# Performance work log

Measured on AMD Instinct MI355X. Metric: run time of the kernel, lower is better.

The kernel has to match this reference:

```python
import jax, jax.numpy as jnp
import numpy as np

B, T, I, H = 64, 1024, 256, 512


def setup_inputs() -> dict:
    key = jax.random.key(0)
    ks = jax.random.split(key, 5)
    s = 1.0 / np.sqrt(H)  # PyTorch LSTM init scale (uniform(-s, s)); we use scaled normal
    return {
        "x": jax.random.normal(ks[0], (B, T, I), dtype=jnp.float32),
        "w_ih": jax.random.normal(ks[1], (4 * H, I), dtype=jnp.float32) * s,
        "w_hh": jax.random.normal(ks[2], (4 * H, H), dtype=jnp.float32) * s,
        "b_ih": jax.random.normal(ks[3], (4 * H,), dtype=jnp.float32) * s,
        "b_hh": jax.random.normal(ks[4], (4 * H,), dtype=jnp.float32) * s,
    }


def _lstm(x, w_ih, w_hh, b_ih, b_hh):
    # x: [B, T, I]. Precompute input projections for all timesteps at once.
    pre = jnp.einsum("bti,gi->btg", x, w_ih) + b_ih + b_hh  # [B, T, 4H]
    pre = jnp.swapaxes(pre, 0, 1)  # [T, B, 4H] for scan over time

    h0 = jnp.zeros((x.shape[0], H), dtype=x.dtype)
    c0 = jnp.zeros((x.shape[0], H), dtype=x.dtype)

    def step(carry, pre_t):
        h, c = carry
        gates = pre_t + h @ w_hh.T  # [B, 4H]
        i, f, g, o = jnp.split(gates, 4, axis=-1)  # PyTorch gate order: i, f, g, o
        i = jax.nn.sigmoid(i)
        f = jax.nn.sigmoid(f)
        g = jnp.tanh(g)
        o = jax.nn.sigmoid(o)
        c = f * c + i * g
        h = o * jnp.tanh(c)
        return (h, c), h

    (h_n, c_n), hs = jax.lax.scan(step, (h0, c0), pre)
    out = jnp.swapaxes(hs, 0, 1)  # [B, T, H] (batch_first=True)
    return out, (h_n[None], c_n[None])  # h_n/c_n: [num_layers=1, B, H]


def reference(x, w_ih, w_hh, b_ih, b_hh):
    return _lstm(x, w_ih, w_hh, b_ih, b_hh)
```

## Files before the change

kernel.cpp:

```cpp
#include <hip/hip_runtime.h>
#include <cstdint>
#include <cstddef>


#define NBATCH 64
#define TSTEPS 1024
#define IDIM   256
#define HDIM   512
#define KDIM   768
#define WS     776
#define ABUF_USHORT (16 * WS)
#define BIAS_OFF    (2 * ABUF_USHORT * 2)
#define SMEM_BYTES  (BIAS_OFF + 1024)

#define HB_WORDS 32768

typedef __attribute__((ext_vector_type(8))) short short8x;
typedef __attribute__((ext_vector_type(4))) float f32x4;
typedef __attribute__((ext_vector_type(4))) unsigned int u32x4;

__device__ __forceinline__ float sigmoid_f(float v) {
    return 1.0f / (1.0f + __expf(-v));
}
__device__ __forceinline__ float tanh_f(float v) {
    float a = fabsf(v);
    float e = __expf(-2.0f * a);
    float r = (1.0f - e) / (1.0f + e);
    return v >= 0.0f ? r : -r;
}
__device__ __forceinline__ unsigned short f2bf(float f) {
    unsigned int u = __float_as_uint(f);
    return (unsigned short)((u + 0x7fffu + ((u >> 16) & 1u)) >> 16);
}
__device__ __forceinline__ unsigned long long pack4(float4 v) {
    unsigned long long b0 = f2bf(v.x), b1 = f2bf(v.y), b2 = f2bf(v.z), b3 = f2bf(v.w);
    return b0 | (b1 << 16) | (b2 << 32) | (b3 << 48);
}
__device__ __forceinline__ unsigned int pklo(unsigned int a, unsigned int b) {
    return (a & 0xffffu) | (b << 16);
}

__global__ void __launch_bounds__(256, 1) lstm_persistent(
    const float* __restrict__ x,
    const float* __restrict__ w_ih,
    const float* __restrict__ w_hh,
    const float* __restrict__ b_ih,
    const float* __restrict__ b_hh,
    float* __restrict__ out,
    unsigned int* __restrict__ h_tb)
{
    const int tid = threadIdx.x;
    const int wg  = blockIdx.x;
    const int bg  = wg >> 3;
    const int hg  = wg & 7;

    extern __shared__ char smem[];
    unsigned short* a0 = (unsigned short*)smem;
    unsigned short* a1 = a0 + ABUF_USHORT;
    float* bias_s = (float*)(smem + BIAS_OFF);

    const int wv   = tid >> 6;
    const int lane = tid & 63;
    const int ln   = lane & 15;
    const int q    = lane >> 4;

    short8x af0[24], af1[24], af2[24], af3[24];
    {
        const int grb = (ln & 3) * HDIM + hg * 64 + wv * 16 + (ln >> 2) * 4;
#define LOADW(AF, TAU)                                                        \
        {                                                                     \
            const int gr = grb + (TAU);                                       \
            _Pragma("unroll")                                                 \
            for (int s = 0; s < 24; ++s) {                                    \
                const float* src = (s < 8)                                    \
                    ? (w_ih + (size_t)gr * IDIM + (s * 32 + q * 8))           \
                    : (w_hh + (size_t)gr * HDIM + ((s - 8) * 32 + q * 8));    \
                float4 v0 = *(const float4*)(src);                            \
                float4 v1 = *(const float4*)(src + 4);                        \
                union { short8x v; unsigned long long u[2]; } tmp;            \
                tmp.u[0] = pack4(v0);                                         \
                tmp.u[1] = pack4(v1);                                         \
                AF[s] = tmp.v;                                                \
            }                                                                 \
        }
        LOADW(af0, 0) LOADW(af1, 1) LOADW(af2, 2) LOADW(af3, 3)
#undef LOADW
    }

    if (ln < 4) {
        const int tau = ln;
        const int hid = hg * 64 + wv * 16 + q * 4 + tau;
        #pragma unroll
        for (int j = 0; j < 4; ++j)
            bias_s[(wv * 4 + q) * 16 + tau * 4 + j] =
                b_ih[j * HDIM + hid] + b_hh[j * HDIM + hid];
    }

    const int sn  = tid >> 4;
    const int sj  = tid & 15;
    const int gbn = bg * 16 + sn;
    const float* xbase = x + (size_t)gbn * TSTEPS * IDIM + sj * 16;

    const size_t hb_off = (size_t)(bg * 16 + ln) * HDIM + hg * 64 + wv * 16 + q * 4;
    float c0 = 0.f, c1 = 0.f, c2 = 0.f, c3 = 0.f;
    float hf0 = 0.f, hf1 = 0.f, hf2 = 0.f, hf3 = 0.f;

    for (int t = 0; t < TSTEPS; ++t) {
        unsigned short* abuf = (t & 1) ? a1 : a0;
        unsigned short* axp  = abuf + sn * WS + sj * 16;
        unsigned int*   ahp32 = (unsigned int*)(abuf + sn * WS + IDIM + sj * 32);

        {
            const float* xp = xbase + (size_t)t * IDIM;
            float4 v0 = *(const float4*)(xp);
            float4 v1 = *(const float4*)(xp + 4);
            float4 v2 = *(const float4*)(xp + 8);
            float4 v3 = *(const float4*)(xp + 12);
            *(unsigned long long*)(axp + 0)  = pack4(v0);
            *(unsigned long long*)(axp + 4)  = pack4(v1);
            *(unsigned long long*)(axp + 8)  = pack4(v2);
            *(unsigned long long*)(axp + 12) = pack4(v3);
        }

        if (t > 0) {
            const unsigned int* hp =
                h_tb + (size_t)(t & 1) * HB_WORDS + (size_t)gbn * HDIM + sj * 32;
            u32x4 hv[8];
            const unsigned int tagw = (unsigned int)t << 16;
            unsigned pend = 0xffu;
            while (pend) {
                #pragma unroll
                for (int u = 0; u < 8; ++u) {
                    if (pend & (1u << u)) {
                        asm volatile("global_load_dwordx4 %0, %1, off sc0 sc1"
                                     : "=v"(hv[u]) : "v"(hp + u * 4) : "memory");
                    }
                }
                asm volatile("s_waitcnt vmcnt(0)" ::: "memory");
                __builtin_amdgcn_sched_barrier(0);
                unsigned np = 0;
                #pragma unroll
                for (int u = 0; u < 8; ++u) {
                    if (pend & (1u << u)) {
                        unsigned m = ((hv[u][0] ^ tagw) | (hv[u][1] ^ tagw) |
                                      (hv[u][2] ^ tagw) | (hv[u][3] ^ tagw))
                                     & 0xffff0000u;
                        if (m) np |= (1u << u);
                    }
                }
                pend = np;
            }
            #pragma unroll
            for (int v = 0; v < 4; ++v) {
                u32x4 a = hv[2 * v], b = hv[2 * v + 1];
                u32x4 w4;
                w4[0] = pklo(a[0], a[1]);
                w4[1] = pklo(a[2], a[3]);
                w4[2] = pklo(b[0], b[1]);
                w4[3] = pklo(b[2], b[3]);
                *(u32x4*)(ahp32 + 4 * v) = w4;
            }
            if ((sn & 7) == ((hg + t) & 7)) {
                float* op = out + ((size_t)gbn * TSTEPS + (t - 1)) * HDIM + sj * 32;
                #pragma unroll
                for (int u = 0; u < 8; ++u) {
                    u32x4 h4 = hv[u];
                    f32x4 f4;
                    f4[0] = __uint_as_float(h4[0] << 16);
                    f4[1] = __uint_as_float(h4[1] << 16);
                    f4[2] = __uint_as_float(h4[2] << 16);
                    f4[3] = __uint_as_float(h4[3] << 16);
                    __builtin_nontemporal_store(f4, (f32x4*)(op + 4 * u));
                }
            }
        } else {
            u32x4 z = {0u, 0u, 0u, 0u};
            #pragma unroll
            for (int v = 0; v < 4; ++v) *(u32x4*)(ahp32 + 4 * v) = z;
        }
        __syncthreads();

        const unsigned short* Bbase = abuf + (size_t)ln * WS + q * 8;
        f32x4 ac0 = {0.f, 0.f, 0.f, 0.f};
        f32x4 ac1 = {0.f, 0.f, 0.f, 0.f};
        f32x4 ac2 = {0.f, 0.f, 0.f, 0.f};
        f32x4 ac3 = {0.f, 0.f, 0.f, 0.f};
        #pragma unroll
        for (int s = 0; s < 24; ++s) {
            short8x bf = *(const short8x*)(Bbase + s * 32);
            ac0 = __builtin_amdgcn_mfma_f32_16x16x32_bf16(af0[s], bf, ac0, 0, 0, 0);
            ac1 = __builtin_amdgcn_mfma_f32_16x16x32_bf16(af1[s], bf, ac1, 0, 0, 0);
            ac2 = __builtin_amdgcn_mfma_f32_16x16x32_bf16(af2[s], bf, ac2, 0, 0, 0);
            ac3 = __builtin_amdgcn_mfma_f32_16x16x32_bf16(af3[s], bf, ac3, 0, 0, 0);
        }

        const unsigned int tagw1 = (unsigned int)(t + 1) << 16;
        const float* bsl = bias_s + (wv * 4 + q) * 16;
        u32x4 pub;
#define ACT(ACC, TAU, CREF, HREF)                                             \
        {                                                                     \
            f32x4 bs = *(const f32x4*)(bsl + (TAU) * 4);                      \
            float ig = sigmoid_f(ACC[0] + bs[0]);                             \
            float fg = sigmoid_f(ACC[1] + bs[1]);                             \
            float gt = tanh_f   (ACC[2] + bs[2]);                             \
            float og = sigmoid_f(ACC[3] + bs[3]);                             \
            CREF = fg * CREF + ig * gt;                                       \
            HREF = og * tanh_f(CREF);                                         \
            pub[TAU] = tagw1 | (unsigned int)f2bf(HREF);                      \
        }
        ACT(ac0, 0, c0, hf0)
        ACT(ac1, 1, c1, hf1)
        ACT(ac2, 2, c2, hf2)
        ACT(ac3, 3, c3, hf3)
#undef ACT
        {
            unsigned int* hb = h_tb + (size_t)((t + 1) & 1) * HB_WORDS + hb_off;
            asm volatile("global_store_dwordx4 %0, %1, off sc0 sc1"
                         :: "v"(hb), "v"(pub) : "memory");
        }
    }

    {
        const size_t HN_OFF = (size_t)NBATCH * TSTEPS * HDIM;
        const size_t CN_OFF = HN_OFF + (size_t)NBATCH * HDIM;
        const int gb   = bg * 16 + ln;
        const int hid0 = hg * 64 + wv * 16 + q * 4;
        f32x4 hv4 = {hf0, hf1, hf2, hf3};
        f32x4 cv4 = {c0, c1, c2, c3};
        *(f32x4*)(out + ((size_t)gb * TSTEPS + (TSTEPS - 1)) * HDIM + hid0) = hv4;
        *(f32x4*)(out + HN_OFF + (size_t)gb * HDIM + hid0) = hv4;
        *(f32x4*)(out + CN_OFF + (size_t)gb * HDIM + hid0) = cv4;
    }
}

extern "C" void kernel_launch(void* const* d_in, const int* in_sizes, int n_in,
                              void* d_out, int out_size, void* d_ws, size_t ws_size,
                              hipStream_t stream) {
    const float* x    = (const float*)d_in[0];
    const float* w_ih = (const float*)d_in[1];
    const float* w_hh = (const float*)d_in[2];
    const float* b_ih = (const float*)d_in[3];
    const float* b_hh = (const float*)d_in[4];
    float* out = (float*)d_out;

    unsigned int* h_tb = (unsigned int*)d_ws;

    (void)hipFuncSetAttribute((const void*)lstm_persistent,
                        hipFuncAttributeMaxDynamicSharedMemorySize, SMEM_BYTES);

    void* args[] = {(void*)&x, (void*)&w_ih, (void*)&w_hh, (void*)&b_ih,
                    (void*)&b_hh, (void*)&out, (void*)&h_tb};
    hipError_t err = hipLaunchCooperativeKernel((void*)lstm_persistent,
                                                dim3(32), dim3(256), args,
                                                SMEM_BYTES, stream);
    if (err != hipSuccess) {
        hipLaunchKernelGGL(lstm_persistent, dim3(32), dim3(256), SMEM_BYTES,
                           stream, x, w_ih, w_hh, b_ih, b_hh, out, h_tb);
    }
}
```

Before: 5.357 ms.

## Overlap x loads with h polling, defer output stores, use hardware exp/rcp/cvt

The x-row loads for the step are now issued as raw asm before the spin-wait on the peer h values, so their latency overlaps the polling, and the bf16 packing happens after a shared waitcnt. Writing h to the output is moved after the h publish and reads back from LDS, taking it off the critical path between the poll and the MFMA. Sigmoid and tanh use exp2/rcp intrinsics, and bf16 conversion uses v_cvt_pk_bf16_f32. The cheaper activations lose some precision, and the tanh form can produce NaN/inf edge behaviour for large inputs, though exp2 saturation usually handles this.

```diff
diff --git a/kernel.cpp b/kernel.cpp
--- a/kernel.cpp
+++ b/kernel.cpp
@@ -7,7 +7,6 @@
 #define TSTEPS 1024
 #define IDIM   256
 #define HDIM   512
-#define KDIM   768
 #define WS     776
 #define ABUF_USHORT (16 * WS)
 #define BIAS_OFF    (2 * ABUF_USHORT * 2)
@@ -20,13 +19,12 @@
 typedef __attribute__((ext_vector_type(4))) unsigned int u32x4;
 
 __device__ __forceinline__ float sigmoid_f(float v) {
-    return 1.0f / (1.0f + __expf(-v));
+    float e = __builtin_amdgcn_exp2f(v * -1.442695040888963f);
+    return __builtin_amdgcn_rcpf(1.0f + e);
 }
 __device__ __forceinline__ float tanh_f(float v) {
-    float a = fabsf(v);
-    float e = __expf(-2.0f * a);
-    float r = (1.0f - e) / (1.0f + e);
-    return v >= 0.0f ? r : -r;
+    float e = __builtin_amdgcn_exp2f(v * 2.885390081777927f);
+    return 1.0f - 2.0f * __builtin_amdgcn_rcpf(e + 1.0f);
 }
 __device__ __forceinline__ unsigned short f2bf(float f) {
     unsigned int u = __float_as_uint(f);
@@ -36,9 +34,16 @@
     unsigned long long b0 = f2bf(v.x), b1 = f2bf(v.y), b2 = f2bf(v.z), b3 = f2bf(v.w);
     return b0 | (b1 << 16) | (b2 << 32) | (b3 << 48);
 }
+__device__ __forceinline__ unsigned int cvtpk_bf16(float a, float b) {
+    unsigned int r;
+    asm("v_cvt_pk_bf16_f32 %0, %1, %2" : "=v"(r) : "v"(a), "v"(b));
+    return r;
+}
 __device__ __forceinline__ unsigned int pklo(unsigned int a, unsigned int b) {
     return (a & 0xffffu) | (b << 16);
 }
+__device__ __forceinline__ float bf_lo(unsigned int w) { return __uint_as_float(w << 16); }
+__device__ __forceinline__ float bf_hi(unsigned int w) { return __uint_as_float(w & 0xffff0000u); }
 
 __global__ void __launch_bounds__(256, 1) lstm_persistent(
     const float* __restrict__ x,
@@ -106,21 +111,16 @@
     float hf0 = 0.f, hf1 = 0.f, hf2 = 0.f, hf3 = 0.f;
 
     for (int t = 0; t < TSTEPS; ++t) {
-        unsigned short* abuf = (t & 1) ? a1 : a0;
-        unsigned short* axp  = abuf + sn * WS + sj * 16;
+        unsigned short* abuf  = (t & 1) ? a1 : a0;
+        unsigned short* axp   = abuf + sn * WS + sj * 16;
         unsigned int*   ahp32 = (unsigned int*)(abuf + sn * WS + IDIM + sj * 32);
 
-        {
-            const float* xp = xbase + (size_t)t * IDIM;
-            float4 v0 = *(const float4*)(xp);
-            float4 v1 = *(const float4*)(xp + 4);
-            float4 v2 = *(const float4*)(xp + 8);
-            float4 v3 = *(const float4*)(xp + 12);
-            *(unsigned long long*)(axp + 0)  = pack4(v0);
-            *(unsigned long long*)(axp + 4)  = pack4(v1);
-            *(unsigned long long*)(axp + 8)  = pack4(v2);
-            *(unsigned long long*)(axp + 12) = pack4(v3);
-        }
+        const float* xp = xbase + (size_t)t * IDIM;
+        f32x4 xv0, xv1, xv2, xv3;
+        asm volatile("global_load_dwordx4 %0, %1, off"           : "=v"(xv0) : "v"(xp));
+        asm volatile("global_load_dwordx4 %0, %1, off offset:16" : "=v"(xv1) : "v"(xp));
+        asm volatile("global_load_dwordx4 %0, %1, off offset:32" : "=v"(xv2) : "v"(xp));
+        asm volatile("global_load_dwordx4 %0, %1, off offset:48" : "=v"(xv3) : "v"(xp));
 
         if (t > 0) {
             const unsigned int* hp =
@@ -129,13 +129,14 @@
             const unsigned int tagw = (unsigned int)t << 16;
             unsigned pend = 0xffu;
             while (pend) {
-                #pragma unroll
-                for (int u = 0; u < 8; ++u) {
-                    if (pend & (1u << u)) {
-                        asm volatile("global_load_dwordx4 %0, %1, off sc0 sc1"
-                                     : "=v"(hv[u]) : "v"(hp + u * 4) : "memory");
-                    }
-                }
+#define POLL1(U, OFF)                                                         \
+                if (pend & (1u << U))                                         \
+                    asm volatile("global_load_dwordx4 %0, %1, off offset:" OFF \
+                                 " sc0 sc1"                                   \
+                                 : "=v"(hv[U]) : "v"(hp) : "memory");
+                POLL1(0, "0")  POLL1(1, "16") POLL1(2, "32") POLL1(3, "48")
+                POLL1(4, "64") POLL1(5, "80") POLL1(6, "96") POLL1(7, "112")
+#undef POLL1
                 asm volatile("s_waitcnt vmcnt(0)" ::: "memory");
                 __builtin_amdgcn_sched_barrier(0);
                 unsigned np = 0;
@@ -160,23 +161,27 @@
                 w4[3] = pklo(b[2], b[3]);
                 *(u32x4*)(ahp32 + 4 * v) = w4;
             }
-            if ((sn & 7) == ((hg + t) & 7)) {
-                float* op = out + ((size_t)gbn * TSTEPS + (t - 1)) * HDIM + sj * 32;
-                #pragma unroll
-                for (int u = 0; u < 8; ++u) {
-                    u32x4 h4 = hv[u];
-                    f32x4 f4;
-                    f4[0] = __uint_as_float(h4[0] << 16);
-                    f4[1] = __uint_as_float(h4[1] << 16);
-                    f4[2] = __uint_as_float(h4[2] << 16);
-                    f4[3] = __uint_as_float(h4[3] << 16);
-                    __builtin_nontemporal_store(f4, (f32x4*)(op + 4 * u));
-                }
-            }
         } else {
             u32x4 z = {0u, 0u, 0u, 0u};
             #pragma unroll
             for (int v = 0; v < 4; ++v) *(u32x4*)(ahp32 + 4 * v) = z;
+        }
+
+        asm volatile("s_waitcnt vmcnt(0)" ::: "memory");
+        __builtin_amdgcn_sched_barrier(0);
+        {
+            unsigned int* axp32 = (unsigned int*)axp;
+            u32x4 xa, xb;
+            xa[0] = cvtpk_bf16(xv0[0], xv0[1]);
+            xa[1] = cvtpk_bf16(xv0[2], xv0[3]);
+            xa[2] = cvtpk_bf16(xv1[0], xv1[1]);
+            xa[3] = cvtpk_bf16(xv1[2], xv1[3]);
+            xb[0] = cvtpk_bf16(xv2[0], xv2[1]);
+            xb[1] = cvtpk_bf16(xv2[2], xv2[3]);
+            xb[2] = cvtpk_bf16(xv3[0], xv3[1]);
+            xb[3] = cvtpk_bf16(xv3[2], xv3[3]);
+            *(u32x4*)(axp32)     = xa;
+            *(u32x4*)(axp32 + 4) = xb;
         }
         __syncthreads();
 
@@ -206,7 +211,7 @@
             float og = sigmoid_f(ACC[3] + bs[3]);                             \
             CREF = fg * CREF + ig * gt;                                       \
             HREF = og * tanh_f(CREF);                                         \
-            pub[TAU] = tagw1 | (unsigned int)f2bf(HREF);                      \
+            pub[TAU] = tagw1 | (cvtpk_bf16(HREF, HREF) & 0xffffu);            \
         }
         ACT(ac0, 0, c0, hf0)
         ACT(ac1, 1, c1, hf1)
@@ -217,6 +222,21 @@
             unsigned int* hb = h_tb + (size_t)((t + 1) & 1) * HB_WORDS + hb_off;
             asm volatile("global_store_dwordx4 %0, %1, off sc0 sc1"
                          :: "v"(hb), "v"(pub) : "memory");
+        }
+
+        if (t > 0 && (sn & 7) == ((hg + t) & 7)) {
+            float* op = out + ((size_t)gbn * TSTEPS + (t - 1)) * HDIM + sj * 32;
+            #pragma unroll
+            for (int v = 0; v < 4; ++v) {
+                u32x4 w4 = *(const u32x4*)(ahp32 + 4 * v);
+                f32x4 o0, o1;
+                o0[0] = bf_lo(w4[0]); o0[1] = bf_hi(w4[0]);
+                o0[2] = bf_lo(w4[1]); o0[3] = bf_hi(w4[1]);
+                o1[0] = bf_lo(w4[2]); o1[1] = bf_hi(w4[2]);
+                o1[2] = bf_lo(w4[3]); o1[3] = bf_hi(w4[3]);
+                __builtin_nontemporal_store(o0, (f32x4*)(op + 8 * v));
+                __builtin_nontemporal_store(o1, (f32x4*)(op + 8 * v + 4));
+            }
         }
     }
 
```

New measurement: 5.142 ms. 1.04x faster.
